# Optimization experiments

Hardware: AMD Instinct MI355X
Metric: run time of the kernel (lower is better)

The kernel has to match this reference:

```python
import jax, jax.numpy as jnp
import numpy as np

N_NODES = 100000
EPS = 1e-12


def gcn_conv(x, src, dst, ew, W, b, n):
    """PyG GCNConv with edge weights: add self-loops (w=1), symmetric norm,
    scatter-add messages from src to dst, then bias."""
    loop = jnp.arange(n)
    src2 = jnp.concatenate([src, loop])
    dst2 = jnp.concatenate([dst, loop])
    ew2 = jnp.concatenate([ew, jnp.ones((n,), dtype=ew.dtype)])
    deg = jax.ops.segment_sum(ew2, dst2, num_segments=n)
    dinv = jnp.where(deg > 0, jax.lax.rsqrt(jnp.where(deg > 0, deg, 1.0)), 0.0)
    norm = dinv[src2] * ew2 * dinv[dst2]  # [E+N]
    xw = x @ W.T                           # [N, H]
    msg = xw[src2] * norm[:, None]         # [E+N, H]  (memory-bound gather)
    out = jax.ops.segment_sum(msg, dst2, num_segments=n)
    return out + b


def setup_inputs() -> dict:
    key = jax.random.key(0)
    ks = jax.random.split(key, 12)
    N, E, D_IN, H, FE = N_NODES, 1600000, 256, 128, 8
    x = jax.random.normal(ks[0], (N, D_IN), dtype=jnp.float32)
    edge_index = jax.random.randint(ks[1], (2, E), 0, N, dtype=jnp.int64)
    edge_attr = jax.random.uniform(ks[2], (E, FE), dtype=jnp.float32)
    s_in = 1.0 / np.sqrt(D_IN)
    s_h = 1.0 / np.sqrt(H)
    W_in = jax.random.uniform(ks[3], (H, D_IN), minval=-s_in, maxval=s_in)
    b_in = jax.random.uniform(ks[4], (H,), minval=-s_in, maxval=s_in)
    W1 = jax.random.uniform(ks[5], (H, H), minval=-s_h, maxval=s_h)
    b1 = jax.random.uniform(ks[6], (H,), minval=-s_h, maxval=s_h)
    W2 = jax.random.uniform(ks[7], (H, H), minval=-s_h, maxval=s_h)
    b2 = jax.random.uniform(ks[8], (H,), minval=-s_h, maxval=s_h)
    W_out = jax.random.uniform(ks[9], (H, H), minval=-s_h, maxval=s_h)
    b_out = jax.random.uniform(ks[10], (H,), minval=-s_h, maxval=s_h)
    return {"x": x, "edge_index": edge_index, "edge_attr": edge_attr,
            "W_in": W_in, "b_in": b_in, "W1": W1, "b1": b1,
            "W2": W2, "b2": b2, "W_out": W_out, "b_out": b_out}


def reference(x, edge_index, edge_attr, W_in, b_in, W1, b1, W2, b2, W_out, b_out):
    n = x.shape[0]
    src, dst = edge_index[0], edge_index[1]
    # edge weights: sum over edge features, then L2-normalize over edges
    ew = edge_attr.sum(axis=1)
    ew = ew / jnp.maximum(jnp.linalg.norm(ew), EPS)
    h = jax.nn.relu(x @ W_in.T + b_in)      # dropout = identity (eval)
    h = jax.nn.relu(gcn_conv(h, src, dst, ew, W1, b1, n))
    h = gcn_conv(h, src, dst, ew, W2, b2, n)
    return h @ W_out.T + b_out
```

## Files before the change

### kernel.cpp

```cpp
#include <hip/hip_runtime.h>
#include <hip/hip_bf16.h>
#include <math.h>


#define CAP 64
#define BN 256
#define BCAP 5120
#define CHUNK 4096
#define SRC_MASK 0x1FFFFu
#define Q_SCALE 16777216.0f
#define Q_INV   5.9604644775390625e-8f
#define GSTRIDE 1024

typedef __attribute__((ext_vector_type(8))) short bf16x8;
typedef __attribute__((ext_vector_type(2))) float f32x2;
typedef __attribute__((ext_vector_type(4))) float f32x4;
typedef __attribute__((ext_vector_type(4))) unsigned int u32x4;

#if __has_builtin(__builtin_amdgcn_cvt_pk_f32_fp8)
#define DEC_SCALE 5.9604644775390625e-8f
__device__ __forceinline__ f32x2 dec2(unsigned short t) {
  return __builtin_amdgcn_cvt_pk_f32_fp8((int)(unsigned)t, false);
}
#else
#define DEC_SCALE 7.922816251426434e28f
__device__ __forceinline__ f32x2 dec2(unsigned short t) {
  f32x2 r;
  r.x = __builtin_bit_cast(float, (((unsigned)t & 0x80u) << 24) | (((unsigned)t & 0x7Fu) << 20));
  r.y = __builtin_bit_cast(float, (((unsigned)t & 0x8000u) << 16) | (((unsigned)t & 0x7F00u) << 12));
  return r;
}
#endif

__device__ __forceinline__ unsigned rne_bf16(float f) {
  const unsigned u = __builtin_bit_cast(unsigned, f);
  return (u + 0x7FFFu + ((u >> 16) & 1u)) >> 16;
}
__device__ __forceinline__ unsigned packsplit(float f) {
  const unsigned hb = rne_bf16(f);
  const float hf = __builtin_bit_cast(float, hb << 16);
  const unsigned lb = rne_bf16(f - hf);
  return (hb << 16) | (lb & 0xFFFFu);
}
__device__ __forceinline__ float unpk(unsigned p) {
  return __builtin_bit_cast(float, p & 0xFFFF0000u) +
         __builtin_bit_cast(float, p << 16);
}
__device__ __forceinline__ void split8(const f32x4 a, const f32x4 b,
                                       bf16x8& hi, bf16x8& lo) {
#pragma unroll
  for (int i = 0; i < 8; ++i) {
    const float f = (i < 4) ? a[i] : b[i - 4];
    const unsigned hb = rne_bf16(f);
    hi[i] = (short)hb;
    const float hf = __builtin_bit_cast(float, hb << 16);
    lo[i] = (short)rne_bf16(f - hf);
  }
}
__device__ __forceinline__ unsigned char enc_e4m3(float v) {
  const float a = v * 0x1p-120f;
  unsigned bits = __builtin_bit_cast(unsigned, a);
  const unsigned sgn = (bits >> 24) & 0x80u;
  bits &= 0x7FFFFFFFu;
  unsigned u7 = (bits + 0x7FFFFu + ((bits >> 20) & 1u)) >> 20;
  if (u7 > 0x7Eu) u7 = 0x7Eu;
  return (unsigned char)(sgn | u7);
}

__global__ void ew_wsplit_kernel(const float* __restrict__ ea, float* __restrict__ ew,
                                 float* __restrict__ partial, int E,
                                 const float* __restrict__ W_in, const float* __restrict__ W1,
                                 const float* __restrict__ W2, const float* __restrict__ W_out,
                                 short* __restrict__ whi, short* __restrict__ wlo) {
  __shared__ float red[256];
  const int tid = threadIdx.x;
  if (blockIdx.x < 1024) {
    float ss = 0.f;
    const int stride = 1024 * 256;
    for (int e = blockIdx.x * 256 + tid; e < E; e += stride) {
      const float4 a = *(const float4*)(ea + (size_t)e * 8);
      const float4 b = *(const float4*)(ea + (size_t)e * 8 + 4);
      const float s = ((a.x + a.y) + (a.z + a.w)) + ((b.x + b.y) + (b.z + b.w));
      ew[e] = s;
      ss = fmaf(s, s, ss);
    }
    red[tid] = ss;
    __syncthreads();
    for (int k = 128; k > 0; k >>= 1) {
      if (tid < k) red[tid] += red[tid + k];
      __syncthreads();
    }
    if (tid == 0) partial[blockIdx.x] = red[0];
  } else {
    const int i = (blockIdx.x - 1024) * 256 + tid;
    if (i < 81920) {
      float f;
      if (i < 32768) f = W_in[i];
      else if (i < 49152) f = W1[i - 32768];
      else if (i < 65536) f = W2[i - 49152];
      else f = W_out[i - 65536];
      const unsigned hb = rne_bf16(f);
      whi[i] = (short)hb;
      wlo[i] = (short)rne_bf16(f - __builtin_bit_cast(float, hb << 16));
    }
  }
}

__global__ void norm_cursor_kernel(const float* __restrict__ partial,
                                   float* __restrict__ invnorm,
                                   unsigned* __restrict__ cursors, int NB) {
  __shared__ float red[256];
  const int tid = threadIdx.x;
  if (blockIdx.x == 0) {
    float s = partial[tid] + partial[tid + 256] + partial[tid + 512] + partial[tid + 768];
    red[tid] = s;
    __syncthreads();
    for (int k = 128; k > 0; k >>= 1) {
      if (tid < k) red[tid] += red[tid + k];
      __syncthreads();
    }
    if (tid == 0) invnorm[0] = 1.0f / fmaxf(sqrtf(red[0]), 1e-12f);
  } else {
    const int i = (blockIdx.x - 1) * 256 + tid;
    if (i < NB) cursors[i * 16] = (unsigned)i * BCAP;
  }
}

__global__ __launch_bounds__(512, 4) void bin_gemmin_kernel(
    const int* __restrict__ src, const int* __restrict__ dst,
    const float* __restrict__ ew, const float* __restrict__ invnorm,
    unsigned* __restrict__ cursors, unsigned long long* __restrict__ buckets,
    int E, int NB, int nbin,
    const float* __restrict__ X, const short* __restrict__ Whi,
    const short* __restrict__ Wlo, const float* __restrict__ bias,
    unsigned* __restrict__ Ypk, int ntiles) {
  __shared__ __align__(16) char smem[36864];
  const int tid = threadIdx.x;
  if ((int)blockIdx.x < nbin) {
    unsigned long long* recs = (unsigned long long*)smem;
    unsigned* hist = (unsigned*)(smem + 32768);
    unsigned* base = (unsigned*)(smem + 34816);
    const int e0 = blockIdx.x * CHUNK;
    const int n = min(CHUNK, E - e0);
    for (int i = tid; i < NB; i += 512) hist[i] = 0;
    __syncthreads();
    const float inv = invnorm[0];
    for (int i = tid; i < n; i += 512) {
      const int s = src[e0 + i];
      const int d = dst[e0 + i];
      const float w = ew[e0 + i] * inv;
      const unsigned q = (unsigned)fminf(fmaf(w, Q_SCALE, 0.5f), 32767.0f);
      recs[i] = ((unsigned long long)(((unsigned)d << 15) | q) << 32) | (unsigned)s;
      atomicAdd(&hist[d >> 8], 1u);
    }
    __syncthreads();
    for (int i = tid; i < NB; i += 512) {
      const unsigned c = hist[i];
      base[i] = c ? atomicAdd(&cursors[i * 16], c) : 0u;
      hist[i] = 0;
    }
    __syncthreads();
    for (int i = tid; i < n; i += 512) {
      const unsigned long long r = recs[i];
      const unsigned b = ((unsigned)(r >> 32) >> 15) >> 8;
      const unsigned pos = base[b] + atomicAdd(&hist[b], 1u);
      if (pos < (b + 1) * BCAP) buckets[pos] = r;
    }
  } else {
    constexpr int K = 256, KT = 8, RT = 2, CPR = 32;
    short* hi_p = (short*)smem;
    short* lo_p = (short*)(smem + 16384);
    const int lane = tid & 63, wave = tid >> 6;
    const int lrow = lane & 15, loct = lane >> 4;

    bf16x8 bhi[KT], blo[KT];
    const int col = wave * 16 + lrow;
#pragma unroll
    for (int kt = 0; kt < KT; ++kt) {
      const int off = col * K + kt * 32 + loct * 8;
      bhi[kt] = *(const bf16x8*)&Whi[off];
      blo[kt] = *(const bf16x8*)&Wlo[off];
    }
    const float bv = bias[col];

    const int r0c = tid >> 5, r1c = (tid + 512) >> 5;
    const int cc = tid & 31;
    f32x4 sa[2][2];
    const int vb = (int)blockIdx.x - nbin;

    int t = vb;
    {
      const int tl = (t < ntiles) ? t : 0;
      const float* xp0 = X + ((size_t)tl * 32 + r0c) * K + cc * 8;
      const float* xp1 = X + ((size_t)tl * 32 + r1c) * K + cc * 8;
      sa[0][0] = *(const f32x4*)xp0; sa[0][1] = *(const f32x4*)(xp0 + 4);
      sa[1][0] = *(const f32x4*)xp1; sa[1][1] = *(const f32x4*)(xp1 + 4);
    }
    while (t < ntiles) {
      {
        const int slot0 = r0c * CPR + (cc ^ (r0c & 7));
        const int slot1 = r1c * CPR + (cc ^ (r1c & 7));
        bf16x8 h, l;
        split8(sa[0][0], sa[0][1], h, l);
        *(bf16x8*)&hi_p[slot0 * 8] = h;
        *(bf16x8*)&lo_p[slot0 * 8] = l;
        split8(sa[1][0], sa[1][1], h, l);
        *(bf16x8*)&hi_p[slot1 * 8] = h;
        *(bf16x8*)&lo_p[slot1 * 8] = l;
      }
      __syncthreads();
      const int tn = t + GSTRIDE;
      {
        const int tl = (tn < ntiles) ? tn : 0;
        const float* xp0 = X + ((size_t)tl * 32 + r0c) * K + cc * 8;
        const float* xp1 = X + ((size_t)tl * 32 + r1c) * K + cc * 8;
        sa[0][0] = *(const f32x4*)xp0; sa[0][1] = *(const f32x4*)(xp0 + 4);
        sa[1][0] = *(const f32x4*)xp1; sa[1][1] = *(const f32x4*)(xp1 + 4);
      }
      f32x4 acc[RT];
#pragma unroll
      for (int rt = 0; rt < RT; ++rt) acc[rt] = f32x4{0.f, 0.f, 0.f, 0.f};
#pragma unroll
      for (int kt = 0; kt < KT; ++kt) {
        bf16x8 ahi[RT], alo[RT];
#pragma unroll
        for (int rt = 0; rt < RT; ++rt) {
          const int lr = rt * 16 + lrow;
          const int off = (lr * CPR + ((kt * 4 + loct) ^ (lr & 7))) * 8;
          ahi[rt] = *(const bf16x8*)&hi_p[off];
          alo[rt] = *(const bf16x8*)&lo_p[off];
        }
#pragma unroll
        for (int rt = 0; rt < RT; ++rt) {
          acc[rt] = __builtin_amdgcn_mfma_f32_16x16x32_bf16(ahi[rt], bhi[kt], acc[rt], 0, 0, 0);
          acc[rt] = __builtin_amdgcn_mfma_f32_16x16x32_bf16(ahi[rt], blo[kt], acc[rt], 0, 0, 0);
          acc[rt] = __builtin_amdgcn_mfma_f32_16x16x32_bf16(alo[rt], bhi[kt], acc[rt], 0, 0, 0);
        }
      }
      const int rbase = t * 32;
#pragma unroll
      for (int rt = 0; rt < RT; ++rt)
#pragma unroll
        for (int r = 0; r < 4; ++r) {
          const float v = fmaxf(acc[rt][r] + bv, 0.f);
          Ypk[(size_t)(rbase + rt * 16 + loct * 4 + r) * 128 + col] = packsplit(v);
        }
      t = tn;
      __syncthreads();
    }
  }
}

__global__ __launch_bounds__(256) void build_kernel(
    const unsigned long long* __restrict__ buckets,
    const unsigned* __restrict__ cursors,
    unsigned* __restrict__ cv, float* __restrict__ dinv,
    int* __restrict__ fillg, int N) {
  __shared__ unsigned cvl[BN * CAP];
  __shared__ unsigned fl[BN];
  const int tid = threadIdx.x;
  const int b = blockIdx.x;
  const int n0 = b << 8;
  for (int i = tid; i < BN * CAP; i += 256) cvl[i] = 0;
  for (int i = tid; i < BN; i += 256) fl[i] = 0;
  __syncthreads();
  const unsigned start = (unsigned)b * BCAP;
  const int cnt = min((int)(cursors[b * 16] - start), BCAP);
  for (int i = tid; i < cnt; i += 256) {
    const unsigned long long r = buckets[start + i];
    const unsigned hi = (unsigned)(r >> 32);
    const unsigned dlo = (hi >> 15) & (BN - 1);
    const unsigned q = hi & 0x7FFFu;
    const unsigned p = atomicAdd(&fl[dlo], 1u);
    if (p < CAP) cvl[(dlo << 6) + p] = (q << 17) | (unsigned)(r & 0xFFFFFFFFu);
  }
  __syncthreads();
  if (n0 + tid < N) {
    const int c = min((int)fl[tid], CAP);
    unsigned qs = 0;
    for (int i = 0; i < c; ++i) qs += cvl[(tid << 6) + i] >> 17;
    dinv[n0 + tid] = rsqrtf(fmaf((float)qs, Q_INV, 1.0f));
    fillg[n0 + tid] = c;
  }
  const u32x4* s = (const u32x4*)cvl;
  u32x4* g = (u32x4*)(cv + ((size_t)b << 14));
  for (int i = tid; i < BN * CAP / 4; i += 256)
    __builtin_nontemporal_store(s[i], &g[i]);
}

template <bool OUT_FP8, bool OUT_F32, bool HAS_BIAS, bool RELU>
__device__ __forceinline__ void gemm_pk_body(
    char* smem, int vb, int stride,
    const unsigned* __restrict__ Xpk, const short* __restrict__ Whi,
    const short* __restrict__ Wlo, const float* __restrict__ bias,
    unsigned* __restrict__ Ypk, unsigned char* __restrict__ Yf8,
    float* __restrict__ Yf32, int ntiles) {
  constexpr int K = 128, KT = 4, CT = 2, RT = 2, CPR = 16;
  short* hi_p = (short*)smem;
  short* lo_p = (short*)(smem + 8192);
  const int tid = threadIdx.x;
  const int lane = tid & 63, wave = tid >> 6;
  const int lrow = lane & 15, loct = lane >> 4;

  bf16x8 bhi[CT][KT], blo[CT][KT];
#pragma unroll
  for (int ct = 0; ct < CT; ++ct) {
    const int col = (wave * CT + ct) * 16 + lrow;
#pragma unroll
    for (int kt = 0; kt < KT; ++kt) {
      const int off = col * K + kt * 32 + loct * 8;
      bhi[ct][kt] = *(const bf16x8*)&Whi[off];
      blo[ct][kt] = *(const bf16x8*)&Wlo[off];
    }
  }
  float bv[CT];
  if constexpr (HAS_BIAS) {
#pragma unroll
    for (int ct = 0; ct < CT; ++ct) bv[ct] = bias[(wave * CT + ct) * 16 + lrow];
  }

  const int r0c = tid >> 4, r1c = (tid + 256) >> 4;
  const int cc = tid & 15;
  u32x4 sa[2][2];

  int t = vb;
  {
    const int tl = (t < ntiles) ? t : 0;
    const unsigned* xp0 = Xpk + ((size_t)tl * 32 + r0c) * K + cc * 8;
    const unsigned* xp1 = Xpk + ((size_t)tl * 32 + r1c) * K + cc * 8;
    sa[0][0] = *(const u32x4*)xp0; sa[0][1] = *(const u32x4*)(xp0 + 4);
    sa[1][0] = *(const u32x4*)xp1; sa[1][1] = *(const u32x4*)(xp1 + 4);
  }
  while (t < ntiles) {
#pragma unroll
    for (int p = 0; p < 2; ++p) {
      const int r = p ? r1c : r0c;
      const int slot = r * CPR + (cc ^ (r & 7));
      const u32x4 a = sa[p][0], b = sa[p][1];
      u32x4 wh, wl;
      wh[0] = (a[1] & 0xFFFF0000u) | (a[0] >> 16);
      wh[1] = (a[3] & 0xFFFF0000u) | (a[2] >> 16);
      wh[2] = (b[1] & 0xFFFF0000u) | (b[0] >> 16);
      wh[3] = (b[3] & 0xFFFF0000u) | (b[2] >> 16);
      wl[0] = (a[1] << 16) | (a[0] & 0xFFFFu);
      wl[1] = (a[3] << 16) | (a[2] & 0xFFFFu);
      wl[2] = (b[1] << 16) | (b[0] & 0xFFFFu);
      wl[3] = (b[3] << 16) | (b[2] & 0xFFFFu);
      *(u32x4*)&hi_p[slot * 8] = wh;
      *(u32x4*)&lo_p[slot * 8] = wl;
    }
    __syncthreads();
    const int tn = t + stride;
    {
      const int tl = (tn < ntiles) ? tn : 0;
      const unsigned* xp0 = Xpk + ((size_t)tl * 32 + r0c) * K + cc * 8;
      const unsigned* xp1 = Xpk + ((size_t)tl * 32 + r1c) * K + cc * 8;
      sa[0][0] = *(const u32x4*)xp0; sa[0][1] = *(const u32x4*)(xp0 + 4);
      sa[1][0] = *(const u32x4*)xp1; sa[1][1] = *(const u32x4*)(xp1 + 4);
    }
    f32x4 acc[RT][CT];
#pragma unroll
    for (int rt = 0; rt < RT; ++rt)
#pragma unroll
      for (int ct = 0; ct < CT; ++ct) acc[rt][ct] = f32x4{0.f, 0.f, 0.f, 0.f};
#pragma unroll
    for (int kt = 0; kt < KT; ++kt) {
      bf16x8 ahi[RT], alo[RT];
#pragma unroll
      for (int rt = 0; rt < RT; ++rt) {
        const int lr = rt * 16 + lrow;
        const int off = (lr * CPR + ((kt * 4 + loct) ^ (lr & 7))) * 8;
        ahi[rt] = *(const bf16x8*)&hi_p[off];
        alo[rt] = *(const bf16x8*)&lo_p[off];
      }
#pragma unroll
      for (int rt = 0; rt < RT; ++rt)
#pragma unroll
        for (int ct = 0; ct < CT; ++ct) {
          acc[rt][ct] = __builtin_amdgcn_mfma_f32_16x16x32_bf16(ahi[rt], bhi[ct][kt], acc[rt][ct], 0, 0, 0);
          acc[rt][ct] = __builtin_amdgcn_mfma_f32_16x16x32_bf16(ahi[rt], blo[ct][kt], acc[rt][ct], 0, 0, 0);
          acc[rt][ct] = __builtin_amdgcn_mfma_f32_16x16x32_bf16(alo[rt], bhi[ct][kt], acc[rt][ct], 0, 0, 0);
        }
    }
    const int rbase = t * 32;
#pragma unroll
    for (int rt = 0; rt < RT; ++rt)
#pragma unroll
      for (int ct = 0; ct < CT; ++ct) {
        const int col = (wave * CT + ct) * 16 + lrow;
#pragma unroll
        for (int r = 0; r < 4; ++r) {
          float v = acc[rt][ct][r];
          if constexpr (HAS_BIAS) v += bv[ct];
          if constexpr (RELU) v = fmaxf(v, 0.f);
          const size_t idx = (size_t)(rbase + rt * 16 + loct * 4 + r) * 128 + col;
          if constexpr (OUT_F32) {
            Yf32[idx] = v;
          } else {
            Ypk[idx] = packsplit(v);
            if constexpr (OUT_FP8) Yf8[idx] = enc_e4m3(v);
          }
        }
      }
    t = tn;
    __syncthreads();
  }
}

__global__ __launch_bounds__(256, 4) void valfin_gemmpk_kernel(
    unsigned* __restrict__ cv, const int* __restrict__ fillg,
    const float* __restrict__ dinv, int N,
    const unsigned* __restrict__ Xpk, const short* __restrict__ Whi,
    const short* __restrict__ Wlo, unsigned* __restrict__ Ypk,
    unsigned char* __restrict__ Yf8, int ntiles) {
  __shared__ __align__(16) char smem[16384];
  if (blockIdx.x < 512) {
    const int total = N * (CAP / 4);
    for (int i = blockIdx.x * 256 + threadIdx.x; i < total; i += 512 * 256) {
      const int n = i >> 4;
      const int slot0 = (i & 15) * 4;
      const int c = fillg[n];
      if (slot0 >= c) continue;
      const float dn = dinv[n];
      u32x4 q = *(u32x4*)&cv[((size_t)n << 6) + slot0];
#pragma unroll
      for (int j = 0; j < 4; ++j) {
        if (slot0 + j < c) {
          const unsigned s = q[j] & SRC_MASK;
          const float wv = dinv[s] * dn * ((float)(q[j] >> 17) * Q_INV);
          const unsigned w15 = (unsigned)fminf(fmaf(wv, Q_SCALE, 0.5f), 32767.0f);
          q[j] = (w15 << 17) | s;
        }
      }
      *(u32x4*)&cv[((size_t)n << 6) + slot0] = q;
    }
  } else {
    gemm_pk_body<true, false, false, false>(smem, (int)blockIdx.x - 512, GSTRIDE,
                                            Xpk, Whi, Wlo, nullptr, Ypk, Yf8,
                                            nullptr, ntiles);
  }
}

template <bool OUT_FP8, bool OUT_F32, bool HAS_BIAS, bool RELU>
__global__ __launch_bounds__(256, 4) void gemm_pk_pipe(
    const unsigned* __restrict__ Xpk, const short* __restrict__ Whi,
    const short* __restrict__ Wlo, const float* __restrict__ bias,
    unsigned* __restrict__ Ypk, unsigned char* __restrict__ Yf8,
    float* __restrict__ Yf32, int ntiles) {
  __shared__ __align__(16) char smem[16384];
  gemm_pk_body<OUT_FP8, OUT_F32, HAS_BIAS, RELU>(smem, (int)blockIdx.x, GSTRIDE,
                                                 Xpk, Whi, Wlo, bias, Ypk, Yf8,
                                                 Yf32, ntiles);
}

template <bool RELU>
__global__ __launch_bounds__(256) void gather_kernel(const unsigned* __restrict__ xw,
                                                     const unsigned char* __restrict__ xf8,
                                                     const int* __restrict__ fill,
                                                     const unsigned* __restrict__ cv,
                                                     const float* __restrict__ dinv,
                                                     const float* __restrict__ bias,
                                                     unsigned* __restrict__ out, int N) {
  const int lane = threadIdx.x & 63;
  const int n = (blockIdx.x * blockDim.x + threadIdx.x) >> 6;
  if (n >= N) return;
  const int f = lane * 2;
  const float dn = dinv[n];
  const float dn2 = dn * dn;
  const uint2 xs = *(const uint2*)&xw[(size_t)n * 128 + f];
  float ax = dn2 * unpk(xs.x);
  float ay = dn2 * unpk(xs.y);
  const unsigned* row = cv + ((size_t)n << 6);
  const int c = min(fill[n], CAP);
  for (int e = 0; e < c; e += 8) {
    const u32x4 ca = *(const u32x4*)&row[e];
    const u32x4 cb = *(const u32x4*)&row[e + 4];
    unsigned cr[8];
    cr[0] = ca[0]; cr[1] = ca[1]; cr[2] = ca[2]; cr[3] = ca[3];
    cr[4] = cb[0]; cr[5] = cb[1]; cr[6] = cb[2]; cr[7] = cb[3];
    unsigned short t[8];
#pragma unroll
    for (int j = 0; j < 8; ++j)
      t[j] = *(const unsigned short*)&xf8[(size_t)(cr[j] & SRC_MASK) * 128 + f];
#pragma unroll
    for (int j = 0; j < 8; ++j) {
      const float vs = (float)(cr[j] >> 17) * DEC_SCALE;
      const f32x2 xy = dec2(t[j]);
      ax = fmaf(vs, xy.x, ax);
      ay = fmaf(vs, xy.y, ay);
    }
  }
  const float2 bb = *(const float2*)&bias[f];
  float o0 = ax + bb.x, o1 = ay + bb.y;
  if (RELU) { o0 = fmaxf(o0, 0.f); o1 = fmaxf(o1, 0.f); }
  uint2 res;
  res.x = packsplit(o0);
  res.y = packsplit(o1);
  *(uint2*)&out[(size_t)n * 128 + f] = res;
}

extern "C" void kernel_launch(void* const* d_in, const int* in_sizes, int n_in,
                              void* d_out, int out_size, void* d_ws, size_t ws_size,
                              hipStream_t stream) {
  const float* x     = (const float*)d_in[0];
  const int*   eidx  = (const int*)d_in[1];
  const float* ea    = (const float*)d_in[2];
  const float* W_in  = (const float*)d_in[3];
  const float* b_in  = (const float*)d_in[4];
  const float* W1    = (const float*)d_in[5];
  const float* b1    = (const float*)d_in[6];
  const float* W2    = (const float*)d_in[7];
  const float* b2    = (const float*)d_in[8];
  const float* W_out = (const float*)d_in[9];
  const float* b_out = (const float*)d_in[10];

  const int E = in_sizes[2] / 8;
  const int N = in_sizes[0] / 256;
  const int* srcp = eidx;
  const int* dstp = eidx + E;
  const int NB = (N + BN - 1) / BN;
  const int nbin = (E + CHUNK - 1) / CHUNK;

  char* w = (char*)d_ws;
  size_t o = 0;
  auto take = [&](size_t bytes) -> void* {
    void* p = w + o;
    o += (bytes + 255) & ~(size_t)255;
    return p;
  };
  float* ew            = (float*)take((size_t)E * 4);
  float* partial       = (float*)take(1024 * 4);
  float* invnorm       = (float*)take(256);
  float* dinv          = (float*)take((size_t)N * 4);
  int*   fillg         = (int*)take((size_t)N * 4);
  short* whi           = (short*)take(81920 * 2);
  short* wlo           = (short*)take(81920 * 2);
  unsigned* cursors    = (unsigned*)take((size_t)NB * 16 * 4);
  unsigned long long* buckets = (unsigned long long*)take((size_t)NB * BCAP * 8);
  unsigned* cv         = (unsigned*)take((size_t)NB * BN * CAP * 4);
  unsigned* buf0       = (unsigned*)take((size_t)N * 128 * 4);
  unsigned* buf1       = (unsigned*)take((size_t)N * 128 * 4);
  unsigned char* buff8 = (unsigned char*)take((size_t)N * 128);
  float* outp          = (float*)d_out;

  const int ntiles = N / 32;

  ew_wsplit_kernel<<<1344, 256, 0, stream>>>(ea, ew, partial, E,
                                             W_in, W1, W2, W_out, whi, wlo);
  norm_cursor_kernel<<<1 + (NB + 255) / 256, 256, 0, stream>>>(partial, invnorm, cursors, NB);
  bin_gemmin_kernel<<<nbin + GSTRIDE, 512, 0, stream>>>(
      srcp, dstp, ew, invnorm, cursors, buckets, E, NB, nbin,
      x, whi, wlo, b_in, buf0, ntiles);
  build_kernel<<<NB, 256, 0, stream>>>(buckets, cursors, cv, dinv, fillg, N);
  valfin_gemmpk_kernel<<<512 + GSTRIDE, 256, 0, stream>>>(
      cv, fillg, dinv, N, buf0, whi + 32768, wlo + 32768, buf1, buff8, ntiles);
  gather_kernel<true><<<(N * 64 + 255) / 256, 256, 0, stream>>>(buf1, buff8, fillg, cv, dinv, b1, buf0, N);
  gemm_pk_pipe<true, false, false, false><<<GSTRIDE, 256, 0, stream>>>(
      buf0, whi + 49152, wlo + 49152, nullptr, buf1, buff8, nullptr, ntiles);
  gather_kernel<false><<<(N * 64 + 255) / 256, 256, 0, stream>>>(buf1, buff8, fillg, cv, dinv, b2, buf0, N);
  gemm_pk_pipe<false, true, true, false><<<GSTRIDE, 256, 0, stream>>>(
      buf0, whi + 65536, wlo + 65536, b_out, nullptr, nullptr, outp, ntiles);
}
```

Measured before the change: 283.6 us.

## Fuse GCN gather aggregation with following dense GEMM into one kernel

Replaces the separate gather kernel and packed GEMM kernel with a single kernel per layer. Each block gathers 32 destination rows into LDS as split bf16 hi/lo pairs, then runs MFMA against register-resident weights and writes the next layer's packed and fp8 outputs. This removes the round trip of the aggregated activations through global memory and one launch per layer. A second fp8 buffer is added so the gather input and GEMM output no longer alias. The cost is lower gather parallelism, since the grid is limited to GSTRIDE persistent blocks and there is a sync per tile.

```diff
diff --git a/kernel.cpp b/kernel.cpp
--- a/kernel.cpp
+++ b/kernel.cpp
@@ -441,62 +441,128 @@
   }
 }
 
-template <bool OUT_FP8, bool OUT_F32, bool HAS_BIAS, bool RELU>
-__global__ __launch_bounds__(256, 4) void gemm_pk_pipe(
-    const unsigned* __restrict__ Xpk, const short* __restrict__ Whi,
-    const short* __restrict__ Wlo, const float* __restrict__ bias,
+template <bool RELU_G, bool OUT_FP8, bool OUT_F32, bool W_BIAS>
+__global__ __launch_bounds__(256, 4) void gather_gemm_kernel(
+    const unsigned* __restrict__ xw, const unsigned char* __restrict__ xf8,
+    const int* __restrict__ fillg, const unsigned* __restrict__ cv,
+    const float* __restrict__ dinv, const float* __restrict__ gbias,
+    const short* __restrict__ Whi, const short* __restrict__ Wlo,
+    const float* __restrict__ wbias,
     unsigned* __restrict__ Ypk, unsigned char* __restrict__ Yf8,
     float* __restrict__ Yf32, int ntiles) {
-  __shared__ __align__(16) char smem[16384];
-  gemm_pk_body<OUT_FP8, OUT_F32, HAS_BIAS, RELU>(smem, (int)blockIdx.x, GSTRIDE,
-                                                 Xpk, Whi, Wlo, bias, Ypk, Yf8,
-                                                 Yf32, ntiles);
-}
-
-template <bool RELU>
-__global__ __launch_bounds__(256) void gather_kernel(const unsigned* __restrict__ xw,
-                                                     const unsigned char* __restrict__ xf8,
-                                                     const int* __restrict__ fill,
-                                                     const unsigned* __restrict__ cv,
-                                                     const float* __restrict__ dinv,
-                                                     const float* __restrict__ bias,
-                                                     unsigned* __restrict__ out, int N) {
-  const int lane = threadIdx.x & 63;
-  const int n = (blockIdx.x * blockDim.x + threadIdx.x) >> 6;
-  if (n >= N) return;
+  constexpr int K = 128, KT = 4, CT = 2, RT = 2, CPR = 16;
+  __shared__ __align__(16) short hi_p[32 * K];
+  __shared__ __align__(16) short lo_p[32 * K];
+  const int tid = threadIdx.x;
+  const int lane = tid & 63, wave = tid >> 6;
+  const int lrow = lane & 15, loct = lane >> 4;
   const int f = lane * 2;
-  const float dn = dinv[n];
-  const float dn2 = dn * dn;
-  const uint2 xs = *(const uint2*)&xw[(size_t)n * 128 + f];
-  float ax = dn2 * unpk(xs.x);
-  float ay = dn2 * unpk(xs.y);
-  const unsigned* row = cv + ((size_t)n << 6);
-  const int c = min(fill[n], CAP);
-  for (int e = 0; e < c; e += 8) {
-    const u32x4 ca = *(const u32x4*)&row[e];
-    const u32x4 cb = *(const u32x4*)&row[e + 4];
-    unsigned cr[8];
-    cr[0] = ca[0]; cr[1] = ca[1]; cr[2] = ca[2]; cr[3] = ca[3];
-    cr[4] = cb[0]; cr[5] = cb[1]; cr[6] = cb[2]; cr[7] = cb[3];
-    unsigned short t[8];
-#pragma unroll
-    for (int j = 0; j < 8; ++j)
-      t[j] = *(const unsigned short*)&xf8[(size_t)(cr[j] & SRC_MASK) * 128 + f];
-#pragma unroll
-    for (int j = 0; j < 8; ++j) {
-      const float vs = (float)(cr[j] >> 17) * DEC_SCALE;
-      const f32x2 xy = dec2(t[j]);
-      ax = fmaf(vs, xy.x, ax);
-      ay = fmaf(vs, xy.y, ay);
-    }
-  }
-  const float2 bb = *(const float2*)&bias[f];
-  float o0 = ax + bb.x, o1 = ay + bb.y;
-  if (RELU) { o0 = fmaxf(o0, 0.f); o1 = fmaxf(o1, 0.f); }
-  uint2 res;
-  res.x = packsplit(o0);
-  res.y = packsplit(o1);
-  *(uint2*)&out[(size_t)n * 128 + f] = res;
+  const int cc8 = lane >> 2;
+  const int ip = (lane & 3) * 2;
+
+  bf16x8 bhi[CT][KT], blo[CT][KT];
+#pragma unroll
+  for (int ct = 0; ct < CT; ++ct) {
+    const int col = (wave * CT + ct) * 16 + lrow;
+#pragma unroll
+    for (int kt = 0; kt < KT; ++kt) {
+      const int off = col * K + kt * 32 + loct * 8;
+      bhi[ct][kt] = *(const bf16x8*)&Whi[off];
+      blo[ct][kt] = *(const bf16x8*)&Wlo[off];
+    }
+  }
+  float wbv[CT];
+  if constexpr (W_BIAS) {
+#pragma unroll
+    for (int ct = 0; ct < CT; ++ct) wbv[ct] = wbias[(wave * CT + ct) * 16 + lrow];
+  }
+  const float2 gb = *(const float2*)&gbias[f];
+
+  for (int t = blockIdx.x; t < ntiles; t += (int)gridDim.x) {
+#pragma unroll
+    for (int pass = 0; pass < 8; ++pass) {
+      const int r = pass * 4 + wave;
+      const int n = t * 32 + r;
+      const float dn = dinv[n];
+      const float dn2 = dn * dn;
+      const uint2 xs = *(const uint2*)&xw[(size_t)n * 128 + f];
+      float ax = dn2 * unpk(xs.x);
+      float ay = dn2 * unpk(xs.y);
+      const unsigned* row = cv + ((size_t)n << 6);
+      const int c = min(fillg[n], CAP);
+      for (int e = 0; e < c; e += 8) {
+        const u32x4 ca = *(const u32x4*)&row[e];
+        const u32x4 cb = *(const u32x4*)&row[e + 4];
+        unsigned cr[8];
+        cr[0] = ca[0]; cr[1] = ca[1]; cr[2] = ca[2]; cr[3] = ca[3];
+        cr[4] = cb[0]; cr[5] = cb[1]; cr[6] = cb[2]; cr[7] = cb[3];
+        unsigned short tb[8];
+#pragma unroll
+        for (int j = 0; j < 8; ++j)
+          tb[j] = *(const unsigned short*)&xf8[(size_t)(cr[j] & SRC_MASK) * 128 + f];
+#pragma unroll
+        for (int j = 0; j < 8; ++j) {
+          const float vs = (float)(cr[j] >> 17) * DEC_SCALE;
+          const f32x2 xy = dec2(tb[j]);
+          ax = fmaf(vs, xy.x, ax);
+          ay = fmaf(vs, xy.y, ay);
+        }
+      }
+      float o0 = ax + gb.x, o1 = ay + gb.y;
+      if constexpr (RELU_G) { o0 = fmaxf(o0, 0.f); o1 = fmaxf(o1, 0.f); }
+      const unsigned h0 = rne_bf16(o0), h1 = rne_bf16(o1);
+      const unsigned l0 = rne_bf16(o0 - __builtin_bit_cast(float, h0 << 16));
+      const unsigned l1 = rne_bf16(o1 - __builtin_bit_cast(float, h1 << 16));
+      const int slot = r * CPR + (cc8 ^ (r & 7));
+      *(unsigned*)&hi_p[slot * 8 + ip] = h0 | (h1 << 16);
+      *(unsigned*)&lo_p[slot * 8 + ip] = l0 | (l1 << 16);
+    }
+    __syncthreads();
+    f32x4 acc[RT][CT];
+#pragma unroll
+    for (int rt = 0; rt < RT; ++rt)
+#pragma unroll
+      for (int ct = 0; ct < CT; ++ct) acc[rt][ct] = f32x4{0.f, 0.f, 0.f, 0.f};
+#pragma unroll
+    for (int kt = 0; kt < KT; ++kt) {
+      bf16x8 ahi[RT], alo[RT];
+#pragma unroll
+      for (int rt = 0; rt < RT; ++rt) {
+        const int lr = rt * 16 + lrow;
+        const int off = (lr * CPR + ((kt * 4 + loct) ^ (lr & 7))) * 8;
+        ahi[rt] = *(const bf16x8*)&hi_p[off];
+        alo[rt] = *(const bf16x8*)&lo_p[off];
+      }
+#pragma unroll
+      for (int rt = 0; rt < RT; ++rt)
+#pragma unroll
+        for (int ct = 0; ct < CT; ++ct) {
+          acc[rt][ct] = __builtin_amdgcn_mfma_f32_16x16x32_bf16(ahi[rt], bhi[ct][kt], acc[rt][ct], 0, 0, 0);
+          acc[rt][ct] = __builtin_amdgcn_mfma_f32_16x16x32_bf16(ahi[rt], blo[ct][kt], acc[rt][ct], 0, 0, 0);
+          acc[rt][ct] = __builtin_amdgcn_mfma_f32_16x16x32_bf16(alo[rt], bhi[ct][kt], acc[rt][ct], 0, 0, 0);
+        }
+    }
+    const int rbase = t * 32;
+#pragma unroll
+    for (int rt = 0; rt < RT; ++rt)
+#pragma unroll
+      for (int ct = 0; ct < CT; ++ct) {
+        const int col = (wave * CT + ct) * 16 + lrow;
+#pragma unroll
+        for (int r = 0; r < 4; ++r) {
+          float v = acc[rt][ct][r];
+          if constexpr (W_BIAS) v += wbv[ct];
+          const size_t idx = (size_t)(rbase + rt * 16 + loct * 4 + r) * 128 + col;
+          if constexpr (OUT_F32) {
+            Yf32[idx] = v;
+          } else {
+            Ypk[idx] = packsplit(v);
+            if constexpr (OUT_FP8) Yf8[idx] = enc_e4m3(v);
+          }
+        }
+      }
+    __syncthreads();
+  }
 }
 
 extern "C" void kernel_launch(void* const* d_in, const int* in_sizes, int n_in,
@@ -540,7 +606,8 @@
   unsigned* cv         = (unsigned*)take((size_t)NB * BN * CAP * 4);
   unsigned* buf0       = (unsigned*)take((size_t)N * 128 * 4);
   unsigned* buf1       = (unsigned*)take((size_t)N * 128 * 4);
-  unsigned char* buff8 = (unsigned char*)take((size_t)N * 128);
+  unsigned char* buff8a = (unsigned char*)take((size_t)N * 128);
+  unsigned char* buff8b = (unsigned char*)take((size_t)N * 128);
   float* outp          = (float*)d_out;
 
   const int ntiles = N / 32;
@@ -553,11 +620,11 @@
       x, whi, wlo, b_in, buf0, ntiles);
   build_kernel<<<NB, 256, 0, stream>>>(buckets, cursors, cv, dinv, fillg, N);
   valfin_gemmpk_kernel<<<512 + GSTRIDE, 256, 0, stream>>>(
-      cv, fillg, dinv, N, buf0, whi + 32768, wlo + 32768, buf1, buff8, ntiles);
-  gather_kernel<true><<<(N * 64 + 255) / 256, 256, 0, stream>>>(buf1, buff8, fillg, cv, dinv, b1, buf0, N);
-  gemm_pk_pipe<true, false, false, false><<<GSTRIDE, 256, 0, stream>>>(
-      buf0, whi + 49152, wlo + 49152, nullptr, buf1, buff8, nullptr, ntiles);
-  gather_kernel<false><<<(N * 64 + 255) / 256, 256, 0, stream>>>(buf1, buff8, fillg, cv, dinv, b2, buf0, N);
-  gemm_pk_pipe<false, true, true, false><<<GSTRIDE, 256, 0, stream>>>(
-      buf0, whi + 65536, wlo + 65536, b_out, nullptr, nullptr, outp, ntiles);
-}
+      cv, fillg, dinv, N, buf0, whi + 32768, wlo + 32768, buf1, buff8a, ntiles);
+  gather_gemm_kernel<true, true, false, false><<<GSTRIDE, 256, 0, stream>>>(
+      buf1, buff8a, fillg, cv, dinv, b1, whi + 49152, wlo + 49152, nullptr,
+      buf0, buff8b, nullptr, ntiles);
+  gather_gemm_kernel<false, false, true, true><<<GSTRIDE, 256, 0, stream>>>(
+      buf0, buff8b, fillg, cv, dinv, b2, whi + 65536, wlo + 65536, b_out,
+      nullptr, nullptr, outp, ntiles);
+}
```

After: 334.9 us. +18.1%, slower.
